# Kernel optimization log

Measured on AMD Instinct MI355X. Metric: run time of the kernel, lower is better.

Reference implementation:

```python
import jax, jax.numpy as jnp
import numpy as np


def setup_inputs() -> dict:
    key = jax.random.key(0)
    k1, k2 = jax.random.split(key)
    n_tokens, embed_dim, num_embed = 16384, 512, 2048
    encode = jax.random.normal(k1, (n_tokens, embed_dim), dtype=jnp.float32)
    # Embedding init in torch: uniform(-1/num_embed, 1/num_embed)
    templat = jax.random.uniform(
        k2, (num_embed, embed_dim), dtype=jnp.float32,
        minval=-1.0 / num_embed, maxval=1.0 / num_embed)
    return {"encode": encode, "templat": templat}


def reference(encode, templat):
    # match_encode_with_templat, eval path: sample=False, detach='encode', metric='l2'
    encode_d = jax.lax.stop_gradient(encode)
    # squared L2 distance: ||e||^2 - 2 e@t^T + ||t||^2 ; logits = -dist
    e_sq = jnp.sum(encode_d * encode_d, axis=-1, keepdims=True)       # (N, 1)
    t_sq = jnp.sum(templat * templat, axis=-1)[None, :]               # (1, M)
    dist = e_sq - 2.0 * (encode_d @ templat.T) + t_sq                 # (N, M)
    logits = -dist
    zsoft = jax.nn.softmax(logits, axis=-1)
    zidx = jnp.argmax(zsoft, axis=-1)                                 # (N,)
    quant = templat[zidx]                                             # (N, C) gather
    return quant, zidx
```

## Files before the change

kernel.cpp:

```cpp
#include <hip/hip_runtime.h>
#include <stdint.h>

#define N_TOK  16384
#define EMB    512
#define NEMB   2048
#define NCHUNK 32
#define CWIN   2.5e-4f

typedef __attribute__((ext_vector_type(8))) short s16x8;
typedef __attribute__((ext_vector_type(4))) float f32x4;

__device__ __forceinline__ unsigned short f2bf(float f) {
  unsigned u = __float_as_uint(f);
  u += 0x7fffu + ((u >> 16) & 1u);
  return (unsigned short)(u >> 16);
}
__device__ __forceinline__ unsigned mapf(float f) {
  unsigned u = __float_as_uint(f);
  return (u >> 31) ? ~u : (u | 0x80000000u);
}
__device__ __forceinline__ float unmapf(unsigned u) {
  return __uint_as_float((u >> 31) ? (u & 0x7fffffffu) : ~u);
}

template<int CTRL>
__device__ __forceinline__ float dppf(float x) {
  return __uint_as_float((unsigned)__builtin_amdgcn_update_dpp(
      0, (int)__float_as_uint(x), CTRL, 0xF, 0xF, true));
}
template<int CTRL>
__device__ __forceinline__ unsigned dppu(unsigned x) {
  return (unsigned)__builtin_amdgcn_update_dpp(0, (int)x, CTRL, 0xF, 0xF, true);
}

__device__ __forceinline__ float pairwise512_sq(const float* se, int lane) {
  int l = lane & 31;
  int b = l >> 3, j = l & 7;
  const float* base = se + b * 128 + j;
  float x = base[0];
  float r = __fmul_rn(x, x);
#pragma unroll
  for (int k = 1; k < 16; ++k) {
    float y = base[8 * k];
    r = __fadd_rn(r, __fmul_rn(y, y));
  }
  r = __fadd_rn(r, __shfl_xor(r, 1));
  r = __fadd_rn(r, __shfl_xor(r, 2));
  r = __fadd_rn(r, __shfl_xor(r, 4));
  r = __fadd_rn(r, __shfl_xor(r, 8));
  r = __fadd_rn(r, __shfl_xor(r, 16));
  return r;
}

__global__ __launch_bounds__(256) void prep_kernel(
    const float* __restrict__ tmp, const float* __restrict__ enc,
    unsigned short* __restrict__ thi, float* __restrict__ tsq,
    unsigned short* __restrict__ ehi, float* __restrict__ esq,
    int* __restrict__ cnt) {
  __shared__ float se[4][EMB];
  int wv = threadIdx.x >> 6, lane = threadIdx.x & 63;
  int row = blockIdx.x * 4 + wv;
  if (blockIdx.x == 0 && threadIdx.x == 0) { cnt[0] = 0; cnt[1] = 0; }
  bool isT = row < NEMB;
  const float* src = isT ? (tmp + (size_t)row * EMB)
                         : (enc + (size_t)(row - NEMB) * EMB);
  const float4* p = (const float4*)src + lane * 2;
  float4 v0 = p[0], v1 = p[1];
  float f[8] = {v0.x, v0.y, v0.z, v0.w, v1.x, v1.y, v1.z, v1.w};
  unsigned h[8];
#pragma unroll
  for (int i = 0; i < 8; ++i) { h[i] = f2bf(f[i]); se[wv][lane * 8 + i] = f[i]; }
  uint4 packed = { h[0] | (h[1] << 16), h[2] | (h[3] << 16),
                   h[4] | (h[5] << 16), h[6] | (h[7] << 16) };
  int lrow = isT ? row : row - NEMB;
  int blk = lrow >> 7, lr = lrow & 127;
  int kt = lane >> 2, cb = (lane & 3) * 16;
  char* base = (char*)(isT ? thi : ehi);
  *(uint4*)(base + (((size_t)(blk * 16 + kt)) << 13) + lr * 64 + cb) = packed;
  __syncthreads();
  float s = pairwise512_sq(se[wv], lane);
  if (lane == 0) { if (isT) tsq[row] = s; else esq[row - NEMB] = s; }
}

__global__ __launch_bounds__(256, 2) void score_kernel(
    const unsigned short* __restrict__ ehi, const unsigned short* __restrict__ thi,
    const float* __restrict__ tsq,
    unsigned long long* __restrict__ keyc, unsigned* __restrict__ s2c) {
  __shared__ __align__(16) char smem[73728];
  const int tid = threadIdx.x, w = tid >> 6, lane = tid & 63;
  const int q = lane >> 4, r = lane & 15;
  const int wr = w >> 1, wc = w & 1;
  const int tokb = (int)blockIdx.x >> 3;
  const int nbp  = (int)blockIdx.x & 7;

  const unsigned short* paA[2];
  const unsigned short* pbB[4];
#pragma unroll
  for (int i = 0; i < 2; ++i) {
    int Lp = i * 4096 + tid * 16;
    int P = Lp ^ (((Lp >> 7) & 3) << 4);
    paA[i] = (const unsigned short*)((const char*)ehi
             + (((size_t)tokb * 16) << 13) + (P >> 6) * 64 + (P & 63));
  }
#pragma unroll
  for (int i = 0; i < 4; ++i) {
    int Lp = i * 4096 + tid * 16;
    int P = Lp ^ (((Lp >> 7) & 3) << 4);
    int sub = P >> 13, rw = (P >> 6) & 127, cbyte = P & 63;
    pbB[i] = (const unsigned short*)((const char*)thi
             + (((size_t)((nbp * 2 + sub) * 16)) << 13) + rw * 64 + cbyte);
  }

#define GLD(src, dst)                                                    \
  __builtin_amdgcn_global_load_lds(                                      \
      (const __attribute__((address_space(1))) void*)(src),              \
      (__attribute__((address_space(3))) void*)(dst), 16, 0, 0)
#define STAGE(t) do {                                                    \
    char* da_ = smem + ((t) % 3) * 8192 + tid * 16;                      \
    char* db_ = smem + 24576 + ((t) % 3) * 16384 + tid * 16;             \
    GLD((const char*)paA[0] + (size_t)(t) * 8192, da_);                  \
    GLD((const char*)paA[1] + (size_t)(t) * 8192, da_ + 4096);           \
    GLD((const char*)pbB[0] + (size_t)(t) * 8192, db_);                  \
    GLD((const char*)pbB[1] + (size_t)(t) * 8192, db_ + 4096);           \
    GLD((const char*)pbB[2] + (size_t)(t) * 8192, db_ + 8192);           \
    GLD((const char*)pbB[3] + (size_t)(t) * 8192, db_ + 12288);          \
  } while (0)

  int offA[4], offB[8];
#pragma unroll
  for (int m = 0; m < 4; ++m) {
    int P = (wr * 64 + m * 16 + r) * 64 + q * 16;
    offA[m] = P ^ (((P >> 7) & 3) << 4);
  }
#pragma unroll
  for (int n = 0; n < 8; ++n) {
    int P = (wc * 128 + n * 16 + r) * 64 + q * 16;
    offB[n] = P ^ (((P >> 7) & 3) << 4);
  }

  f32x4 acc[4][8];
#pragma unroll
  for (int m = 0; m < 4; ++m)
#pragma unroll
    for (int n = 0; n < 8; ++n) acc[m][n] = (f32x4){0.f, 0.f, 0.f, 0.f};

  STAGE(0); STAGE(1);
  asm volatile("s_waitcnt vmcnt(6)" ::: "memory");
  __builtin_amdgcn_s_barrier();

#pragma unroll
  for (int t = 0; t < 16; ++t) {
    const char* Ab_ = smem + (t % 3) * 8192;
    const char* Bb_ = smem + 24576 + (t % 3) * 16384;
    if (t + 2 < 16) STAGE(t + 2);
    s16x8 af[4], bf[8];
#pragma unroll
    for (int m = 0; m < 4; ++m) af[m] = *(const s16x8*)(Ab_ + offA[m]);
#pragma unroll
    for (int n = 0; n < 8; ++n) bf[n] = *(const s16x8*)(Bb_ + offB[n]);
    __builtin_amdgcn_s_setprio(1);
#pragma unroll
    for (int n = 0; n < 8; ++n) {
      acc[0][n] = __builtin_amdgcn_mfma_f32_16x16x32_bf16(af[0], bf[n], acc[0][n], 0, 0, 0);
      acc[1][n] = __builtin_amdgcn_mfma_f32_16x16x32_bf16(af[1], bf[n], acc[1][n], 0, 0, 0);
      acc[2][n] = __builtin_amdgcn_mfma_f32_16x16x32_bf16(af[2], bf[n], acc[2][n], 0, 0, 0);
      acc[3][n] = __builtin_amdgcn_mfma_f32_16x16x32_bf16(af[3], bf[n], acc[3][n], 0, 0, 0);
    }
    __builtin_amdgcn_s_setprio(0);
    if (t < 14) { asm volatile("s_waitcnt vmcnt(6)" ::: "memory"); }
    else        { asm volatile("s_waitcnt vmcnt(0)" ::: "memory"); }
    __builtin_amdgcn_s_barrier();
  }

#define FOLD(CTRL) { float os_ = dppf<CTRL>(sb), os2_ = dppf<CTRL>(s2f);        \
    float mx_ = fmaxf(sb, os_);                                                 \
    s2f = fminf(fminf(s2f, os2_), mx_); sb = fminf(sb, os_); }
#define FOLDL(CTRL) { unsigned ol_ = dppu<CTRL>(li); li = li < ol_ ? li : ol_; }
#pragma unroll
  for (int nh = 0; nh < 2; ++nh) {
    const int chunk = nbp * 4 + wc * 2 + nh;
    const int nbase = chunk * 64;
    const float tq0 = tsq[nbase + r], tq1 = tsq[nbase + 16 + r],
                tq2 = tsq[nbase + 32 + r], tq3 = tsq[nbase + 48 + r];
#pragma unroll
    for (int m = 0; m < 4; ++m) {
      unsigned long long kk[4]; unsigned ss[4];
#pragma unroll
      for (int i = 0; i < 4; ++i) {
        float s0 = fmaf(-2.f, acc[m][nh * 4 + 0][i], tq0);
        float s1 = fmaf(-2.f, acc[m][nh * 4 + 1][i], tq1);
        float s2v = fmaf(-2.f, acc[m][nh * 4 + 2][i], tq2);
        float s3 = fmaf(-2.f, acc[m][nh * 4 + 3][i], tq3);
        float n01 = fminf(s0, s1), X01 = fmaxf(s0, s1);
        float n23 = fminf(s2v, s3), X23 = fmaxf(s2v, s3);
        float sb = fminf(n01, n23);
        float s2f = fminf(fminf(X01, X23), fmaxf(n01, n23));
        FOLD(0xB1) FOLD(0x4E) FOLD(0x124) FOLD(0x128)
        unsigned li = 0xFFFFFFFFu;
        li = (s3  == sb) ? (unsigned)(48 + r) : li;
        li = (s2v == sb) ? (unsigned)(32 + r) : li;
        li = (s1  == sb) ? (unsigned)(16 + r) : li;
        li = (s0  == sb) ? (unsigned)(r)      : li;
        FOLDL(0xB1) FOLDL(0x4E) FOLDL(0x124) FOLDL(0x128)
        kk[i] = ((unsigned long long)mapf(sb) << 32) | (unsigned)(nbase + (int)li);
        ss[i] = mapf(s2f);
      }
      if (r == 0) {
        int token0 = tokb * 128 + wr * 64 + m * 16 + q * 4;
#pragma unroll
        for (int i = 0; i < 4; ++i) {
          keyc[(size_t)(token0 + i) * NCHUNK + chunk] = kk[i];
          s2c [(size_t)(token0 + i) * NCHUNK + chunk] = ss[i];
        }
      }
    }
  }
#undef FOLD
#undef FOLDL
#undef GLD
#undef STAGE
}

__global__ __launch_bounds__(256) void finish_kernel(
    const float* __restrict__ tmp,
    const unsigned long long* __restrict__ keyc, const unsigned* __restrict__ s2c,
    int* __restrict__ work, int* __restrict__ ftok, int* __restrict__ cnt,
    unsigned long long* __restrict__ rkey, float* __restrict__ out) {
  const int wv = threadIdx.x >> 6, lane = threadIdx.x & 63;
  const int t = blockIdx.x * 4 + wv;
  unsigned long long myk = ~0ULL; unsigned mys = 0xffffffffu;
  if (lane < 32) {
    myk = keyc[(size_t)t * NCHUNK + lane];
    mys = s2c[(size_t)t * NCHUNK + lane];
  }
  unsigned long long K = myk; unsigned S = mys;
#pragma unroll
  for (int mask = 1; mask < 32; mask <<= 1) {
    unsigned long long ko = __shfl_xor(K, mask);
    unsigned so = __shfl_xor(S, mask);
    unsigned long long mx = K > ko ? K : ko;
    unsigned hi = (unsigned)(mx >> 32);
    K = K < ko ? K : ko;
    S = S < so ? S : so;
    S = hi < S ? hi : S;
  }
  K = __shfl(K, 0); S = __shfl(S, 0);
  float best_f   = unmapf((unsigned)(K >> 32));
  float second_f = unmapf(S);
  int idx = (int)(unsigned)(K & 0xffffffffu);
  bool ok = (second_f - best_f >= CWIN) && (idx >= 0) && (idx < NEMB) && (best_f == best_f);
  if (!ok) {
    bool nanCase = !(best_f == best_f);
    float limit = best_f + CWIN;
    bool cand = false;
    if (lane < 32) {
      float cf = unmapf((unsigned)(myk >> 32));
      cand = nanCase || !(cf > limit);
    }
    unsigned long long mask = __ballot(cand);
    int base = 0;
    if (lane == 0) base = atomicAdd(&cnt[0], __popcll(mask));
    base = __shfl(base, 0);
    if (cand) {
      int rank = __popcll(mask & ((1ULL << lane) - 1ULL));
      work[base + rank] = t * NCHUNK + lane;
    }
    if (lane == 0) {
      rkey[t] = ~0ULL;
      int fp = atomicAdd(&cnt[1], 1);
      ftok[fp] = t;
    }
    return;
  }
  const float4* src = (const float4*)(tmp + (size_t)idx * EMB) + lane * 2;
  float4* dst = (float4*)(out + (size_t)t * EMB) + lane * 2;
  dst[0] = src[0];
  dst[1] = src[1];
  if (lane == 0) out[(size_t)N_TOK * EMB + t] = (float)idx;
}

__global__ __launch_bounds__(256) void patch_kernel(
    const float* __restrict__ enc, const float* __restrict__ tmp,
    const float* __restrict__ esq, const float* __restrict__ tsq,
    const int* __restrict__ work, const int* __restrict__ cnt,
    unsigned long long* __restrict__ rkey) {
  int total = cnt[0];
  __shared__ float se[EMB];
  __shared__ unsigned long long s_min[4];
  const int tid = threadIdx.x, wv = tid >> 6, lane = tid & 63;
  const int g = lane >> 4, l16 = lane & 15;
  for (int p = blockIdx.x; p < total; p += gridDim.x) {
    __syncthreads();
    int item = work[p];
    int t = item >> 5, c = item & 31;
    const float4* erow = (const float4*)(enc + (size_t)t * EMB);
    for (int i = tid; i < 128; i += 256) ((float4*)se)[i] = erow[i];
    __syncthreads();
    float e2 = esq[t];
    unsigned long long lkey = ~0ULL;
#pragma unroll
    for (int j = 0; j < 4; ++j) {
      int m = c * 64 + wv * 16 + j * 4 + g;
      const float4* trow = (const float4*)(tmp + (size_t)m * EMB);
      double s = 0.0;
#pragma unroll
      for (int k = 0; k < 8; ++k) {
        float4 a = trow[l16 + 16 * k];
        float4 b = ((const float4*)se)[l16 + 16 * k];
        s += (double)a.x * b.x + (double)a.y * b.y
           + (double)a.z * b.z + (double)a.w * b.w;
      }
      s += __shfl_xor(s, 1); s += __shfl_xor(s, 2);
      s += __shfl_xor(s, 4); s += __shfl_xor(s, 8);
      if (l16 == 0) {
        float M  = (float)s;
        float d1 = __fadd_rn(e2, -__fmul_rn(2.0f, M));
        float d2 = __fadd_rn(d1, tsq[m]);
        unsigned long long key =
            ((unsigned long long)__float_as_uint(d2) << 32) | (unsigned)m;
        if (key < lkey) lkey = key;
      }
    }
    { unsigned long long o = __shfl_xor(lkey, 16); lkey = lkey < o ? lkey : o; }
    { unsigned long long o = __shfl_xor(lkey, 32); lkey = lkey < o ? lkey : o; }
    if (lane == 0) s_min[wv] = lkey;
    __syncthreads();
    if (tid == 0) {
      unsigned long long M = s_min[0];
      M = s_min[1] < M ? s_min[1] : M;
      M = s_min[2] < M ? s_min[2] : M;
      M = s_min[3] < M ? s_min[3] : M;
      atomicMin(&rkey[t], M);
    }
  }
}

__global__ __launch_bounds__(256) void fixup_kernel(
    const float* __restrict__ tmp, const int* __restrict__ ftok,
    const int* __restrict__ cnt, const unsigned long long* __restrict__ rkey,
    float* __restrict__ out) {
  int total = cnt[1];
  const int lane = threadIdx.x & 63;
  for (int widx = blockIdx.x * 4 + (threadIdx.x >> 6); widx < total;
       widx += gridDim.x * 4) {
    int t = ftok[widx];
    int idx = (int)(unsigned)(rkey[t] & 0xffffffffULL);
    idx = idx < 0 ? 0 : (idx > NEMB - 1 ? NEMB - 1 : idx);
    const float4* src = (const float4*)(tmp + (size_t)idx * EMB) + lane * 2;
    float4* dst = (float4*)(out + (size_t)t * EMB) + lane * 2;
    dst[0] = src[0];
    dst[1] = src[1];
    if (lane == 0) out[(size_t)N_TOK * EMB + t] = (float)idx;
  }
}

extern "C" void kernel_launch(void* const* d_in, const int* in_sizes, int n_in,
                              void* d_out, int out_size, void* d_ws, size_t ws_size,
                              hipStream_t stream) {
  const float* enc = (const float*)d_in[0];
  const float* tmp = (const float*)d_in[1];
  float* out = (float*)d_out;
  char* ws = (char*)d_ws;
  unsigned short* thi = (unsigned short*)ws;
  unsigned short* ehi = (unsigned short*)(ws + 2097152);
  float* tsq      = (float*)(ws + 18874368);
  float* esq      = (float*)(ws + 18882560);
  unsigned long long* keyc = (unsigned long long*)(ws + 18948096);
  unsigned* s2c   = (unsigned*)(ws + 23142400);
  int*   cnt      = (int*)  (ws + 25239552);
  int*   ftok     = (int*)  (ws + 25239616);
  unsigned long long* rkey = (unsigned long long*)(ws + 25305152);
  int*   work     = (int*)  (ws + 25436224);

  prep_kernel  <<<4608,     256, 0, stream>>>(tmp, enc, thi, tsq, ehi, esq, cnt);
  score_kernel <<<1024,     256, 0, stream>>>(ehi, thi, tsq, keyc, s2c);
  finish_kernel<<<N_TOK/4,  256, 0, stream>>>(tmp, keyc, s2c, work, ftok, cnt, rkey, out);
  patch_kernel <<<2048,     256, 0, stream>>>(enc, tmp, esq, tsq, work, cnt, rkey);
  fixup_kernel <<<1024,     256, 0, stream>>>(tmp, ftok, cnt, rkey, out);
}
```

Baseline: 179.9 us.

## Fuse fixup gather into patch kernel via per-token countdown; remap score block order

After: 213.0 us. 1.18x slower.

```diff
diff --git a/kernel.cpp b/kernel.cpp
--- a/kernel.cpp
+++ b/kernel.cpp
@@ -60,7 +60,7 @@
   __shared__ float se[4][EMB];
   int wv = threadIdx.x >> 6, lane = threadIdx.x & 63;
   int row = blockIdx.x * 4 + wv;
-  if (blockIdx.x == 0 && threadIdx.x == 0) { cnt[0] = 0; cnt[1] = 0; }
+  if (blockIdx.x == 0 && threadIdx.x == 0) cnt[0] = 0;
   bool isT = row < NEMB;
   const float* src = isT ? (tmp + (size_t)row * EMB)
                          : (enc + (size_t)(row - NEMB) * EMB);
@@ -90,8 +90,8 @@
   const int tid = threadIdx.x, w = tid >> 6, lane = tid & 63;
   const int q = lane >> 4, r = lane & 15;
   const int wr = w >> 1, wc = w & 1;
-  const int tokb = (int)blockIdx.x >> 3;
-  const int nbp  = (int)blockIdx.x & 7;
+  const int tokb = (int)blockIdx.x & 127;
+  const int nbp  = (int)blockIdx.x >> 7;
 
   const unsigned short* paA[2];
   const unsigned short* pbB[4];
@@ -224,7 +224,7 @@
 __global__ __launch_bounds__(256) void finish_kernel(
     const float* __restrict__ tmp,
     const unsigned long long* __restrict__ keyc, const unsigned* __restrict__ s2c,
-    int* __restrict__ work, int* __restrict__ ftok, int* __restrict__ cnt,
+    int* __restrict__ work, int* __restrict__ ncand, int* __restrict__ cnt,
     unsigned long long* __restrict__ rkey, float* __restrict__ out) {
   const int wv = threadIdx.x >> 6, lane = threadIdx.x & 63;
   const int t = blockIdx.x * 4 + wv;
@@ -258,8 +258,9 @@
       cand = nanCase || !(cf > limit);
     }
     unsigned long long mask = __ballot(cand);
+    int npop = __popcll(mask);
     int base = 0;
-    if (lane == 0) base = atomicAdd(&cnt[0], __popcll(mask));
+    if (lane == 0) base = atomicAdd(&cnt[0], npop);
     base = __shfl(base, 0);
     if (cand) {
       int rank = __popcll(mask & ((1ULL << lane) - 1ULL));
@@ -267,8 +268,7 @@
     }
     if (lane == 0) {
       rkey[t] = ~0ULL;
-      int fp = atomicAdd(&cnt[1], 1);
-      ftok[fp] = t;
+      ncand[t] = npop;
     }
     return;
   }
@@ -283,10 +283,12 @@
     const float* __restrict__ enc, const float* __restrict__ tmp,
     const float* __restrict__ esq, const float* __restrict__ tsq,
     const int* __restrict__ work, const int* __restrict__ cnt,
-    unsigned long long* __restrict__ rkey) {
+    int* __restrict__ ncand, unsigned long long* __restrict__ rkey,
+    float* __restrict__ out) {
   int total = cnt[0];
   __shared__ float se[EMB];
   __shared__ unsigned long long s_min[4];
+  __shared__ int s_idx;
   const int tid = threadIdx.x, wv = tid >> 6, lane = tid & 63;
   const int g = lane >> 4, l16 = lane & 15;
   for (int p = blockIdx.x; p < total; p += gridDim.x) {
@@ -331,26 +333,22 @@
       M = s_min[2] < M ? s_min[2] : M;
       M = s_min[3] < M ? s_min[3] : M;
       atomicMin(&rkey[t], M);
-    }
-  }
-}
-
-__global__ __launch_bounds__(256) void fixup_kernel(
-    const float* __restrict__ tmp, const int* __restrict__ ftok,
-    const int* __restrict__ cnt, const unsigned long long* __restrict__ rkey,
-    float* __restrict__ out) {
-  int total = cnt[1];
-  const int lane = threadIdx.x & 63;
-  for (int widx = blockIdx.x * 4 + (threadIdx.x >> 6); widx < total;
-       widx += gridDim.x * 4) {
-    int t = ftok[widx];
-    int idx = (int)(unsigned)(rkey[t] & 0xffffffffULL);
-    idx = idx < 0 ? 0 : (idx > NEMB - 1 ? NEMB - 1 : idx);
-    const float4* src = (const float4*)(tmp + (size_t)idx * EMB) + lane * 2;
-    float4* dst = (float4*)(out + (size_t)t * EMB) + lane * 2;
-    dst[0] = src[0];
-    dst[1] = src[1];
-    if (lane == 0) out[(size_t)N_TOK * EMB + t] = (float)idx;
+      __threadfence();
+      int left = atomicSub(&ncand[t], 1);
+      if (left == 1) {
+        unsigned long long K = atomicAdd(&rkey[t], 0ULL);
+        int idx = (int)(unsigned)(K & 0xffffffffULL);
+        s_idx = idx < 0 ? 0 : (idx > NEMB - 1 ? NEMB - 1 : idx);
+      } else s_idx = -1;
+    }
+    __syncthreads();
+    int idx = s_idx;
+    if (idx >= 0) {
+      const float4* srow = (const float4*)(tmp + (size_t)idx * EMB);
+      float4* drow = (float4*)(out + (size_t)t * EMB);
+      for (int i = tid; i < 128; i += 256) drow[i] = srow[i];
+      if (tid == 0) out[(size_t)N_TOK * EMB + t] = (float)idx;
+    }
   }
 }
 
@@ -368,13 +366,12 @@
   unsigned long long* keyc = (unsigned long long*)(ws + 18948096);
   unsigned* s2c   = (unsigned*)(ws + 23142400);
   int*   cnt      = (int*)  (ws + 25239552);
-  int*   ftok     = (int*)  (ws + 25239616);
+  int*   ncand    = (int*)  (ws + 25239616);
   unsigned long long* rkey = (unsigned long long*)(ws + 25305152);
   int*   work     = (int*)  (ws + 25436224);
 
   prep_kernel  <<<4608,     256, 0, stream>>>(tmp, enc, thi, tsq, ehi, esq, cnt);
   score_kernel <<<1024,     256, 0, stream>>>(ehi, thi, tsq, keyc, s2c);
-  finish_kernel<<<N_TOK/4,  256, 0, stream>>>(tmp, keyc, s2c, work, ftok, cnt, rkey, out);
-  patch_kernel <<<2048,     256, 0, stream>>>(enc, tmp, esq, tsq, work, cnt, rkey);
-  fixup_kernel <<<1024,     256, 0, stream>>>(tmp, ftok, cnt, rkey, out);
-}
+  finish_kernel<<<N_TOK/4,  256, 0, stream>>>(tmp, keyc, s2c, work, ncand, cnt, rkey, out);
+  patch_kernel <<<2048,     256, 0, stream>>>(enc, tmp, esq, tsq, work, cnt, ncand, rkey, out);
+}
```
